# Optimization experiments

Hardware: AMD Instinct MI355X
Metric: run time of the kernel (lower is better)

The kernel has to match this reference:

```python
import jax, jax.numpy as jnp
import numpy as np

N = 262144
DX = 126
A_DIM = 2
IN = DX + A_DIM  # 128
Z = 10


def _bn(h, g, b):
    # torch BatchNorm1d in train mode: biased batch stats
    mu = h.mean(0)
    var = h.var(0)
    return g * (h - mu) * jax.lax.rsqrt(var + 1e-5) + b


def _kld(mu_p, ss_p, mu_q, ss_q):
    # KL between diagonal Gaussians per-sample, /dim, mean over batch
    k = mu_p.shape[1]
    kl = 0.5 * (jnp.sum(jnp.log(ss_q) - jnp.log(ss_p) + ss_p / ss_q
                        + (mu_p - mu_q) ** 2 / ss_q, axis=1) - k)
    return jnp.mean(kl / k)


def _sym(mu1, ss1, mu2, ss2):
    return 0.5 * (_kld(mu1, ss1, mu2, ss2) + _kld(mu2, ss2, mu1, ss1))


def _bce(p, t):
    return -jnp.mean(t * jnp.log(p) + (1.0 - t) * jnp.log(1.0 - p))


def _corr(x, y):
    n = x.shape[0]
    xm, ym = x.mean(), y.mean()
    xv = jnp.sum((x - xm) ** 2) / (n - 1)
    yv = jnp.sum((y - ym) ** 2) / (n - 1)
    c = jnp.abs(jnp.sum((x - xm) * (y - ym)) / jnp.sqrt(xv * yv))
    return jnp.where(xm == 0, 0.0, c)


def _twin(z, y, a):
    # fused segmented replacement for the python where/argmax group loops
    gid = y.astype(jnp.int32) * A_DIM + jnp.argmax(a, axis=1).astype(jnp.int32)
    G = 2 * A_DIM
    ones = jnp.ones((z.shape[0],), z.dtype)
    cnt = jax.ops.segment_sum(ones, gid, num_segments=G)
    s1 = jax.ops.segment_sum(z, gid, num_segments=G)
    s2 = jax.ops.segment_sum(z * z, gid, num_segments=G)
    safe = jnp.maximum(cnt, 1.0)[:, None]
    mean = s1 / safe
    var = (s2 - cnt[:, None] * mean ** 2) / jnp.maximum(cnt - 1.0, 1.0)[:, None]
    mean = mean.reshape(2, A_DIM, -1)
    var = var.reshape(2, A_DIM, -1)
    valid = (cnt >= 2).reshape(2, A_DIM)
    d = (jnp.sum((mean[:, :-1] - mean[:, 1:]) ** 2, -1)
         + jnp.sum((var[:, :-1] - var[:, 1:]) ** 2, -1))
    msk = valid[:, :-1] & valid[:, 1:]
    return jnp.sum(jnp.where(msk, d, 0.0))


def _forward(x, a, eps, y, p):
    (W1, b1, g1, be1, g2, be2, W2, b2,
     Wc1, bc1, Wc2, bc2, Wd1, bd1, Wd2, bd2, Wn, bnb) = p
    enc = lambda h: jax.nn.relu(_bn(jax.nn.relu(_bn(h @ W1 + b1, g1, be1)), g2, be2)) @ W2 + b2
    cla = lambda z: (z @ Wc1 + bc1) @ Wc2 + bc2
    dec = lambda z: (z @ Wd1 + bd1) @ Wd2 + bd2
    split = lambda zt: (zt[:, :10], zt[:, 10:20], zt[:, 20:30], zt[:, 30:40])

    def bi_kld(mx1, lx1, ms1, ls1, mx2, lx2, ms2, ls2):
        sx1, ss1 = jnp.exp(lx1), jnp.exp(ls1)
        sx2, ss2 = jnp.exp(lx2), jnp.exp(ls2)
        return (_sym(mx1, sx1, mx2, sx2), _sym(ms1, ss1, ms2, ss2),
                (_sym(mx1, sx1, ms1, ss1), _sym(mx2, sx2, ms2, ss2)))

    # pass 1: encoder on (x,a) / (x,1-a); only zx1/zx2 are used (for y_pred)
    mx1, ms1, lx1, ls1 = split(enc(jnp.concatenate([x, a], 1)))
    mx2, ms2, lx2, ls2 = split(enc(jnp.concatenate([x, 1.0 - a], 1)))
    zx1 = eps[0] * jnp.exp(lx1 / 2) + mx1
    zx2 = eps[2] * jnp.exp(lx2 / 2) + mx2
    y_pred = jnp.argmax(cla(zx1) + cla(zx2), axis=1).astype(x.dtype)[:, None]

    # pass 2: new_net then encoder
    out_o = jax.nn.relu(jnp.concatenate([x, a, y_pred], 1) @ Wn + bnb)
    out_c = jax.nn.relu(jnp.concatenate([x, 1.0 - a, y_pred], 1) @ Wn + bnb)
    mx1, ms1, lx1, ls1 = split(enc(out_o))
    mx2, ms2, lx2, ls2 = split(enc(out_c))
    d_zx, d_zs, (dxs1, dxs2) = bi_kld(mx1, lx1, ms1, ls1, mx2, lx2, ms2, ls2)
    zx1 = eps[4] * jnp.exp(lx1 / 2) + mx1
    zs1 = eps[5] * jnp.exp(ls1 / 2) + ms1
    zx2 = eps[6] * jnp.exp(lx2 / 2) + mx2
    zs2 = eps[7] * jnp.exp(ls2 / 2) + ms2

    r1 = jax.nn.sigmoid(dec(jnp.concatenate([zx1, zs1], 1)))
    r2 = jax.nn.sigmoid(dec(jnp.concatenate([zx2, zs2], 1)))
    x_ori, a_ori = jax.nn.sigmoid(x), jax.nn.sigmoid(a)
    recon_loss = (0.5 * (_bce(r1[:, :-A_DIM], x_ori) + _bce(r2[:, :-A_DIM], x_ori))
                  + 0.5 * (_bce(r1[:, -A_DIM:], a_ori) + _bce(r2[:, -A_DIM:], a_ori)))

    rs1 = jax.nn.sigmoid(dec(jnp.concatenate([zx1, zs2], 1)))
    rs2 = jax.nn.sigmoid(dec(jnp.concatenate([zx2, zs1], 1)))
    sr_loss = 0.5 * (_bce(rs1, jnp.concatenate([x_ori, a_ori], 1))
                     + _bce(rs2, jnp.concatenate([x_ori, jax.nn.sigmoid(1.0 - a)], 1)))

    dis_loss = d_zx + jnp.exp(-d_zs) + jnp.exp(-dxs1) + jnp.exp(-dxs2)
    twin = _twin(zx1, y, a)
    a_tags = jnp.argmax(a, 1).astype(x.dtype)
    yi = y.astype(jnp.int32)[:, None]
    ce = lambda lg: -jnp.take_along_axis(jax.nn.log_softmax(lg, -1), yi, axis=1)[:, 0]
    cl = 0.5 * (ce(cla(zx1)) + ce(cla(zx2)))
    F1 = 1.0  # config.f1
    return (jnp.sum(cl), F1 * _corr(a_tags, cl), 0.1 * twin,
            dis_loss, recon_loss, sr_loss)


def setup_inputs() -> dict:
    key = jax.random.key(0)
    ks = jax.random.split(key, 16)
    w = lambda k, shp: jax.random.normal(k, shp, jnp.float32) * 0.05
    return {
        'x': jax.random.normal(ks[0], (N, DX), jnp.float32),
        'a': jax.random.uniform(ks[1], (N, A_DIM), jnp.float32),
        'eps': jax.random.normal(ks[2], (8, N, Z), jnp.float32),
        'y': jax.random.randint(ks[3], (N,), 0, 2).astype(jnp.int32),
        'W1': w(ks[4], (IN, 128)), 'b1': jnp.zeros(128, jnp.float32),
        'g1': jnp.ones(128, jnp.float32), 'be1': jnp.zeros(128, jnp.float32),
        'g2': jnp.ones(128, jnp.float32), 'be2': jnp.zeros(128, jnp.float32),
        'W2': w(ks[5], (128, 40)), 'b2': jnp.zeros(40, jnp.float32),
        'Wc1': w(ks[6], (Z, 32)), 'bc1': jnp.zeros(32, jnp.float32),
        'Wc2': w(ks[7], (32, 2)), 'bc2': jnp.zeros(2, jnp.float32),
        'Wd1': w(ks[8], (20, 16)), 'bd1': jnp.zeros(16, jnp.float32),
        'Wd2': w(ks[9], (16, IN)), 'bd2': jnp.zeros(IN, jnp.float32),
        'Wn': w(ks[10], (IN + 1, IN)), 'bnb': jnp.zeros(IN, jnp.float32),
    }


def reference(x, a, eps, y, W1, b1, g1, be1, g2, be2, W2, b2,
              Wc1, bc1, Wc2, bc2, Wd1, bd1, Wd2, bd2, Wn, bnb):
    p = (W1, b1, g1, be1, g2, be2, W2, b2,
         Wc1, bc1, Wc2, bc2, Wd1, bd1, Wd2, bd2, Wn, bnb)
    return _forward(x, a, eps, y, p)
```

## Files before the change

kernel.cpp:

```cpp
#include <hip/hip_runtime.h>
#include <hip/hip_bf16.h>
#include <math.h>


#define N_      262144
#define DX_     126

static const size_t OFF_STATS = 0;
static const size_t OFF_PAR   = 32768;
static const size_t OFF_BUFA  = 65536;
static const size_t SZ_NH     = (size_t)N_ * 128 * 4;
static const size_t OFF_BUFB  = OFF_BUFA + SZ_NH;
static const size_t OFF_E1    = OFF_BUFB + SZ_NH;
static const size_t OFF_E2    = OFF_E1 + (size_t)N_*40*4;
static const size_t OFF_ZX1   = OFF_E2 + (size_t)N_*40*4;
static const size_t OFF_ZS1   = OFF_ZX1 + (size_t)N_*10*4;
static const size_t OFF_ZX2   = OFF_ZS1 + (size_t)N_*10*4;
static const size_t OFF_ZS2   = OFF_ZX2 + (size_t)N_*10*4;
static const size_t OFF_YP    = OFF_ZS2 + (size_t)N_*10*4;

#define ST_P1BN1    0
#define ST_P1BN2    512
#define ST_P2BN1    1024
#define ST_P2BN2    1536
#define ST_KLD      2048
#define ST_CL       2052
#define ST_TWIN_CNT 2056
#define ST_TWIN_S1  2060
#define ST_TWIN_S2  2100
#define ST_BCE_PART 2176

#define PP1BN1  0
#define PP1BN2  512
#define PP2BN1  1024
#define PP2BN2  1536

__device__ __forceinline__ float softplus_f(float u) {
    return fmaxf(u, 0.0f) + __logf(1.0f + __expf(-fabsf(u)));
}
__device__ __forceinline__ float sigmoid_f(float u) {
    return __builtin_amdgcn_rcpf(1.0f + __expf(-u));
}

#define BMg 128
#define BKg 32

__global__ __launch_bounds__(256, 4) void gemm_plain_kernel(
    const float* __restrict__ A, int K, const float* __restrict__ W,
    float* __restrict__ C)
{
    __shared__ __align__(16) float As[BKg][BMg + 4];
    __shared__ __align__(16) float Bs[BKg][128];
    const int row0 = blockIdx.x * BMg;
    const int tid  = threadIdx.x;
    const int tr   = (tid / 16) * 8;
    const int tc   = (tid % 16) * 8;
    float acc[8][8] = {};
    const int nk = (K + BKg - 1) / BKg;
    for (int kc = 0; kc < nk; ++kc) {
        const int k0 = kc * BKg;
        #pragma unroll
        for (int i = 0; i < 16; ++i) {
            int idx = tid + i * 256;
            int m = idx / BKg, k = idx % BKg;
            int gk = k0 + k;
            As[k][m] = (gk < K) ? A[(size_t)(row0 + m) * K + gk] : 0.0f;
        }
        #pragma unroll
        for (int i = 0; i < 16; ++i) {
            int idx = tid + i * 256;
            int k = idx / 128, n = idx % 128;
            int gk = k0 + k;
            Bs[k][n] = (gk < K) ? W[(size_t)gk * 128 + n] : 0.0f;
        }
        __syncthreads();
        #pragma unroll
        for (int k = 0; k < BKg; ++k) {
            float4 a0 = *(const float4*)&As[k][tr];
            float4 a1 = *(const float4*)&As[k][tr + 4];
            float4 b0 = *(const float4*)&Bs[k][tc];
            float4 b1v = *(const float4*)&Bs[k][tc + 4];
            float av[8] = {a0.x, a0.y, a0.z, a0.w, a1.x, a1.y, a1.z, a1.w};
            float bv[8] = {b0.x, b0.y, b0.z, b0.w, b1v.x, b1v.y, b1v.z, b1v.w};
            #pragma unroll
            for (int i = 0; i < 8; ++i)
                #pragma unroll
                for (int j = 0; j < 8; ++j)
                    acc[i][j] = fmaf(av[i], bv[j], acc[i][j]);
        }
        __syncthreads();
    }
    #pragma unroll
    for (int i = 0; i < 8; ++i) {
        float4 s0 = {acc[i][0], acc[i][1], acc[i][2], acc[i][3]};
        float4 s1 = {acc[i][4], acc[i][5], acc[i][6], acc[i][7]};
        size_t base = (size_t)(row0 + tr + i) * 128 + tc;
        *(float4*)&C[base]     = s0;
        *(float4*)&C[base + 4] = s1;
    }
}

__global__ __launch_bounds__(256, 4) void gemm_front_kernel(
    const float* U2, const float* __restrict__ a,
    const float* __restrict__ ypred, const float* __restrict__ Wn,
    const float* __restrict__ bnb, int conj,
    const float* __restrict__ W1, const float* __restrict__ b1,
    float* Cout)
{
    __shared__ __align__(16) float As[BKg][BMg + 4];
    __shared__ __align__(16) float Bs[BKg][128];
    __shared__ float ra0[BMg], ra1[BMg], ryp[BMg];
    __shared__ float w6s[128], w7s[128], w8s[128], bns[128];
    const int row0 = blockIdx.x * BMg;
    const int tid  = threadIdx.x;
    if (tid < 128) {
        int r = row0 + tid;
        float a0 = a[2 * r], a1 = a[2 * r + 1];
        if (conj) { a0 = 1.0f - a0; a1 = 1.0f - a1; }
        ra0[tid] = a0; ra1[tid] = a1; ryp[tid] = ypred[r];
        w6s[tid] = Wn[126 * 128 + tid];
        w7s[tid] = Wn[127 * 128 + tid];
        w8s[tid] = Wn[128 * 128 + tid];
        bns[tid] = bnb[tid];
    }
    __syncthreads();
    const int tr = (tid / 16) * 8;
    const int tc = (tid % 16) * 8;
    float acc[8][8] = {};
    for (int kc = 0; kc < 4; ++kc) {
        const int k0 = kc * BKg;
        #pragma unroll
        for (int i = 0; i < 16; ++i) {
            int idx = tid + i * 256;
            int m = idx / BKg, k = idx % BKg;
            int gk = k0 + k;
            float u = U2[(size_t)(row0 + m) * 128 + gk];
            float v = u + ra0[m] * w6s[gk] + ra1[m] * w7s[gk]
                        + ryp[m] * w8s[gk] + bns[gk];
            As[k][m] = fmaxf(v, 0.0f);
        }
        #pragma unroll
        for (int i = 0; i < 16; ++i) {
            int idx = tid + i * 256;
            int k = idx / 128, n = idx % 128;
            Bs[k][n] = W1[(size_t)(k0 + k) * 128 + n];
        }
        __syncthreads();
        #pragma unroll
        for (int k = 0; k < BKg; ++k) {
            float4 a0 = *(const float4*)&As[k][tr];
            float4 a1 = *(const float4*)&As[k][tr + 4];
            float4 b0 = *(const float4*)&Bs[k][tc];
            float4 b1v = *(const float4*)&Bs[k][tc + 4];
            float av[8] = {a0.x, a0.y, a0.z, a0.w, a1.x, a1.y, a1.z, a1.w};
            float bv[8] = {b0.x, b0.y, b0.z, b0.w, b1v.x, b1v.y, b1v.z, b1v.w};
            #pragma unroll
            for (int i = 0; i < 8; ++i)
                #pragma unroll
                for (int j = 0; j < 8; ++j)
                    acc[i][j] = fmaf(av[i], bv[j], acc[i][j]);
        }
        __syncthreads();
    }
    float bias[8];
    #pragma unroll
    for (int j = 0; j < 8; ++j) bias[j] = b1[tc + j];
    #pragma unroll
    for (int i = 0; i < 8; ++i) {
        float4 s0 = {acc[i][0] + bias[0], acc[i][1] + bias[1],
                     acc[i][2] + bias[2], acc[i][3] + bias[3]};
        float4 s1 = {acc[i][4] + bias[4], acc[i][5] + bias[5],
                     acc[i][6] + bias[6], acc[i][7] + bias[7]};
        size_t base = (size_t)(row0 + tr + i) * 128 + tc;
        *(float4*)&Cout[base]     = s0;
        *(float4*)&Cout[base + 4] = s1;
    }
}

__global__ __launch_bounds__(256) void stats_p1_bn1_kernel(
    const float* __restrict__ U1, const float* __restrict__ a,
    const float* __restrict__ W1, const float* __restrict__ b1,
    double* __restrict__ stat)
{
    const int tid = threadIdx.x;
    const int col = tid & 127, half = tid >> 7;
    const int r0 = blockIdx.x * 256 + half * 128;
    const float w6 = W1[126 * 128 + col], w7 = W1[127 * 128 + col];
    const float bb = b1[col];
    double dso = 0, dqo = 0, dsc = 0, dqc = 0;
    for (int i0 = 0; i0 < 128; i0 += 64) {
        float so = 0, qo = 0, sc = 0, qc = 0;
        for (int i = i0; i < i0 + 64; ++i) {
            int r = r0 + i;
            float u  = U1[(size_t)r * 128 + col];
            float a0 = a[2 * r], a1 = a[2 * r + 1];
            float ho = u + a0 * w6 + a1 * w7 + bb;
            float hc = u + (1.0f - a0) * w6 + (1.0f - a1) * w7 + bb;
            so += ho; qo += ho * ho; sc += hc; qc += hc * hc;
        }
        dso += so; dqo += qo; dsc += sc; dqc += qc;
    }
    __shared__ double red[4][128];
    if (half == 1) { red[0][col]=dso; red[1][col]=dqo; red[2][col]=dsc; red[3][col]=dqc; }
    __syncthreads();
    if (half == 0) {
        atomicAdd(&stat[col],       dso + red[0][col]);
        atomicAdd(&stat[128 + col], dqo + red[1][col]);
        atomicAdd(&stat[256 + col], dsc + red[2][col]);
        atomicAdd(&stat[384 + col], dqc + red[3][col]);
    }
}

__global__ __launch_bounds__(256) void stats_p1_bn2_kernel(
    const float* __restrict__ U1, const float* __restrict__ a,
    const float* __restrict__ W1, const float* __restrict__ b1,
    const float* __restrict__ Pbn1, double* __restrict__ stat)
{
    const int tid = threadIdx.x;
    const int col = tid & 127, half = tid >> 7;
    const int r0 = blockIdx.x * 256 + half * 128;
    const float w6 = W1[126 * 128 + col], w7 = W1[127 * 128 + col];
    const float bb = b1[col];
    const float A1o = Pbn1[col],       B1o = Pbn1[128 + col];
    const float A1c = Pbn1[256 + col], B1c = Pbn1[384 + col];
    double dso = 0, dqo = 0, dsc = 0, dqc = 0;
    for (int i0 = 0; i0 < 128; i0 += 64) {
        float so = 0, qo = 0, sc = 0, qc = 0;
        for (int i = i0; i < i0 + 64; ++i) {
            int r = r0 + i;
            float u  = U1[(size_t)r * 128 + col];
            float a0 = a[2 * r], a1 = a[2 * r + 1];
            float ho = u + a0 * w6 + a1 * w7 + bb;
            float hc = u + (1.0f - a0) * w6 + (1.0f - a1) * w7 + bb;
            float r1o = fmaxf(fmaf(A1o, ho, B1o), 0.0f);
            float r1c = fmaxf(fmaf(A1c, hc, B1c), 0.0f);
            so += r1o; qo += r1o * r1o; sc += r1c; qc += r1c * r1c;
        }
        dso += so; dqo += qo; dsc += sc; dqc += qc;
    }
    __shared__ double red[4][128];
    if (half == 1) { red[0][col]=dso; red[1][col]=dqo; red[2][col]=dsc; red[3][col]=dqc; }
    __syncthreads();
    if (half == 0) {
        atomicAdd(&stat[col],       dso + red[0][col]);
        atomicAdd(&stat[128 + col], dqo + red[1][col]);
        atomicAdd(&stat[256 + col], dsc + red[2][col]);
        atomicAdd(&stat[384 + col], dqc + red[3][col]);
    }
}

__global__ __launch_bounds__(256) void stats_p2_bn1_kernel(
    const float* __restrict__ H1o, const float* __restrict__ H1c,
    double* __restrict__ stat)
{
    const int tid = threadIdx.x;
    const int col = tid & 127, br = tid >> 7;
    const float* H = br ? H1c : H1o;
    const int r0 = blockIdx.x * 256;
    double ds = 0, dq = 0;
    for (int i0 = 0; i0 < 256; i0 += 64) {
        float s = 0, q = 0;
        for (int i = i0; i < i0 + 64; ++i) {
            float h = H[(size_t)(r0 + i) * 128 + col];
            s += h; q += h * h;
        }
        ds += s; dq += q;
    }
    atomicAdd(&stat[br * 256 + col], ds);
    atomicAdd(&stat[br * 256 + 128 + col], dq);
}

__global__ __launch_bounds__(256) void stats_p2_bn2_kernel(
    const float* __restrict__ H1o, const float* __restrict__ H1c,
    const float* __restrict__ Pbn1, double* __restrict__ stat)
{
    const int tid = threadIdx.x;
    const int col = tid & 127, br = tid >> 7;
    const float* H = br ? H1c : H1o;
    const float A1 = Pbn1[br * 256 + col], B1 = Pbn1[br * 256 + 128 + col];
    const int r0 = blockIdx.x * 256;
    double ds = 0, dq = 0;
    for (int i0 = 0; i0 < 256; i0 += 64) {
        float s = 0, q = 0;
        for (int i = i0; i < i0 + 64; ++i) {
            float h = H[(size_t)(r0 + i) * 128 + col];
            float r1 = fmaxf(fmaf(A1, h, B1), 0.0f);
            s += r1; q += r1 * r1;
        }
        ds += s; dq += q;
    }
    atomicAdd(&stat[br * 256 + col], ds);
    atomicAdd(&stat[br * 256 + 128 + col], dq);
}

__global__ void finalize_bn_kernel(const double* __restrict__ stat,
                                   const float* __restrict__ g,
                                   const float* __restrict__ be,
                                   float* __restrict__ Pout)
{
    const int br = blockIdx.x, j = threadIdx.x;
    double s = stat[br * 256 + j], q = stat[br * 256 + 128 + j];
    double mu = s / (double)N_;
    double var = q / (double)N_ - mu * mu;
    float rstd = (float)rsqrt(var + 1e-5);
    float A = g[j] * rstd;
    float B = be[j] - (float)mu * A;
    Pout[br * 256 + j] = A;
    Pout[br * 256 + 128 + j] = B;
}

__global__ __launch_bounds__(256) void tail_p1_kernel(
    const float* __restrict__ U1, const float* __restrict__ a, int conj,
    const float* __restrict__ W1, const float* __restrict__ b1,
    const float* __restrict__ A1p, const float* __restrict__ B1p,
    const float* __restrict__ A2p, const float* __restrict__ B2p,
    const float* __restrict__ W2, const float* __restrict__ b2,
    const float* __restrict__ epsk, float* __restrict__ zout)
{
    __shared__ float As[128][69];
    __shared__ float outs[64][24];
    const int row0 = blockIdx.x * 64;
    const int tid  = threadIdx.x;
    for (int i = tid; i < 64 * 128; i += 256) {
        int r = i >> 7, k = i & 127;
        int gr = row0 + r;
        float a0 = a[2 * gr], a1 = a[2 * gr + 1];
        if (conj) { a0 = 1.0f - a0; a1 = 1.0f - a1; }
        float h = U1[(size_t)gr * 128 + k] + a0 * W1[126 * 128 + k]
                + a1 * W1[127 * 128 + k] + b1[k];
        float r1 = fmaxf(fmaf(A1p[k], h, B1p[k]), 0.0f);
        float r2 = fmaxf(fmaf(A2p[k], r1, B2p[k]), 0.0f);
        As[k][r] = r2;
    }
    __syncthreads();
    const int row = tid & 63;
    const int cg  = tid >> 6;
    const int wbase = __builtin_amdgcn_readfirstlane((cg < 2) ? cg * 5 : 10 + cg * 5);
    float acc[5] = {};
    for (int k = 0; k < 128; ++k) {
        float av = As[k][row];
        #pragma unroll
        for (int c = 0; c < 5; ++c)
            acc[c] = fmaf(av, W2[k * 40 + wbase + c], acc[c]);
    }
    #pragma unroll
    for (int c = 0; c < 5; ++c)
        outs[row][cg * 5 + c] = acc[c] + b2[wbase + c];
    __syncthreads();
    if (tid < 128) {
        int r = tid & 63, dg = tid >> 6;
        int gr = row0 + r;
        #pragma unroll
        for (int c = 0; c < 5; ++c) {
            int d = dg * 5 + c;
            float mx = outs[r][d], lx = outs[r][10 + d];
            zout[(size_t)gr * 10 + d] =
                epsk[(size_t)gr * 10 + d] * __expf(0.5f * lx) + mx;
        }
    }
}

__global__ __launch_bounds__(256) void tail_p2_kernel(
    const float* __restrict__ H1,
    const float* __restrict__ A1p, const float* __restrict__ B1p,
    const float* __restrict__ A2p, const float* __restrict__ B2p,
    const float* __restrict__ W2, const float* __restrict__ b2,
    float* __restrict__ E)
{
    __shared__ float As[128][69];
    __shared__ float outs[64][44];
    const int row0 = blockIdx.x * 64;
    const int tid  = threadIdx.x;
    for (int i = tid; i < 64 * 128; i += 256) {
        int r = i >> 7, k = i & 127;
        float h = H1[(size_t)(row0 + r) * 128 + k];
        float r1 = fmaxf(fmaf(A1p[k], h, B1p[k]), 0.0f);
        float r2 = fmaxf(fmaf(A2p[k], r1, B2p[k]), 0.0f);
        As[k][r] = r2;
    }
    __syncthreads();
    const int row = tid & 63;
    const int cg  = tid >> 6;
    const int wbase = __builtin_amdgcn_readfirstlane(cg * 10);
    float acc[10] = {};
    for (int k = 0; k < 128; ++k) {
        float av = As[k][row];
        #pragma unroll
        for (int c = 0; c < 10; ++c)
            acc[c] = fmaf(av, W2[k * 40 + wbase + c], acc[c]);
    }
    #pragma unroll
    for (int c = 0; c < 10; ++c)
        outs[row][wbase + c] = acc[c] + b2[wbase + c];
    __syncthreads();
    size_t base = (size_t)row0 * 40;
    for (int i = tid; i < 64 * 40; i += 256)
        E[base + i] = outs[i / 40][i % 40];
}

__global__ __launch_bounds__(256) void cla_argmax_kernel(
    const float* __restrict__ zx1, const float* __restrict__ zx2,
    const float* __restrict__ Wc1, const float* __restrict__ bc1,
    const float* __restrict__ Wc2, const float* __restrict__ bc2,
    float* __restrict__ ypred)
{
    const int r = blockIdx.x * 256 + threadIdx.x;
    float z1[10], z2[10];
    #pragma unroll
    for (int d = 0; d < 10; ++d) {
        z1[d] = zx1[(size_t)r * 10 + d];
        z2[d] = zx2[(size_t)r * 10 + d];
    }
    float lg0 = 2.0f * bc2[0], lg1 = 2.0f * bc2[1];
    #pragma unroll
    for (int j = 0; j < 32; ++j) {
        float s1 = bc1[j], s2 = bc1[j];
        #pragma unroll
        for (int d = 0; d < 10; ++d) {
            float w = Wc1[d * 32 + j];
            s1 += z1[d] * w; s2 += z2[d] * w;
        }
        float s = s1 + s2;
        lg0 += s * Wc2[j * 2 + 0];
        lg1 += s * Wc2[j * 2 + 1];
    }
    ypred[r] = (lg1 > lg0) ? 1.0f : 0.0f;
}

__device__ __forceinline__ float sym10(const float* m1, const float* l1,
                                       const float* m2, const float* l2)
{
    float t12 = 0, t21 = 0;
    #pragma unroll
    for (int j = 0; j < 10; ++j) {
        float dl = l1[j] - l2[j];
        float md = m1[j] - m2[j]; md *= md;
        t12 += -dl + __expf(dl)  + md * __expf(-l2[j]);
        t21 +=  dl + __expf(-dl) + md * __expf(-l1[j]);
    }
    return 0.025f * ((t12 - 10.0f) + (t21 - 10.0f));
}

__device__ __forceinline__ float ce2_of(const float* z, int yv,
    const float* Wc1, const float* bc1, const float* Wc2, const float* bc2)
{
    float lg0 = bc2[0], lg1 = bc2[1];
    #pragma unroll
    for (int j = 0; j < 32; ++j) {
        float s = bc1[j];
        #pragma unroll
        for (int d = 0; d < 10; ++d) s += z[d] * Wc1[d * 32 + j];
        lg0 += s * Wc2[j * 2 + 0];
        lg1 += s * Wc2[j * 2 + 1];
    }
    float m = fmaxf(lg0, lg1);
    float lse = m + __logf(__expf(lg0 - m) + __expf(lg1 - m));
    float ly = yv ? lg1 : lg0;
    return -(ly - lse);
}

__global__ __launch_bounds__(256) void latents_kernel(
    const float* __restrict__ E1, const float* __restrict__ E2,
    const float* __restrict__ eps,
    const int* __restrict__ y, const float* __restrict__ a,
    const float* __restrict__ Wc1, const float* __restrict__ bc1,
    const float* __restrict__ Wc2, const float* __restrict__ bc2,
    float* __restrict__ zx1, float* __restrict__ zs1,
    float* __restrict__ zx2, float* __restrict__ zs2,
    double* __restrict__ stat)
{
    __shared__ float tw_cnt[4], tw_s1[40], tw_s2[40];
    __shared__ float redw[4][8];
    const int tid = threadIdx.x;
    if (tid < 4) tw_cnt[tid] = 0.0f;
    if (tid < 40) { tw_s1[tid] = 0.0f; tw_s2[tid] = 0.0f; }
    __syncthreads();

    const int r = blockIdx.x * 256 + tid;
    const size_t NS = (size_t)N_ * 10;
    float e1[40], e2[40];
    #pragma unroll
    for (int i = 0; i < 40; ++i) {
        e1[i] = E1[(size_t)r * 40 + i];
        e2[i] = E2[(size_t)r * 40 + i];
    }
    float s_dzx  = sym10(e1 + 0,  e1 + 20, e2 + 0,  e2 + 20);
    float s_dzs  = sym10(e1 + 10, e1 + 30, e2 + 10, e2 + 30);
    float s_dxs1 = sym10(e1 + 0,  e1 + 20, e1 + 10, e1 + 30);
    float s_dxs2 = sym10(e2 + 0,  e2 + 20, e2 + 10, e2 + 30);

    float z1[10], z2[10];
    #pragma unroll
    for (int d = 0; d < 10; ++d) {
        size_t rd = (size_t)r * 10 + d;
        float v1 = eps[4 * NS + rd] * __expf(0.5f * e1[20 + d]) + e1[d];
        float t1 = eps[5 * NS + rd] * __expf(0.5f * e1[30 + d]) + e1[10 + d];
        float v2 = eps[6 * NS + rd] * __expf(0.5f * e2[20 + d]) + e2[d];
        float t2 = eps[7 * NS + rd] * __expf(0.5f * e2[30 + d]) + e2[10 + d];
        zx1[rd] = v1; zs1[rd] = t1; zx2[rd] = v2; zs2[rd] = t2;
        z1[d] = v1; z2[d] = v2;
    }

    const int yv = y[r];
    float ce1 = ce2_of(z1, yv, Wc1, bc1, Wc2, bc2);
    float ce2 = ce2_of(z2, yv, Wc1, bc1, Wc2, bc2);
    float cl = 0.5f * (ce1 + ce2);
    float atag = (a[2 * r + 1] > a[2 * r]) ? 1.0f : 0.0f;

    int gid = yv * 2 + (int)atag;
    atomicAdd(&tw_cnt[gid], 1.0f);
    #pragma unroll
    for (int d = 0; d < 10; ++d) {
        atomicAdd(&tw_s1[gid * 10 + d], z1[d]);
        atomicAdd(&tw_s2[gid * 10 + d], z1[d] * z1[d]);
    }

    float vals[8] = {s_dzx, s_dzs, s_dxs1, s_dxs2, cl, cl * cl, atag * cl, atag};
    #pragma unroll
    for (int v = 0; v < 8; ++v) {
        float sv = vals[v];
        #pragma unroll
        for (int off = 1; off < 64; off <<= 1) sv += __shfl_xor(sv, off);
        vals[v] = sv;
    }
    const int wave = tid >> 6;
    if ((tid & 63) == 0) {
        #pragma unroll
        for (int v = 0; v < 8; ++v) redw[wave][v] = vals[v];
    }
    __syncthreads();
    if (tid < 8) {
        float s = redw[0][tid] + redw[1][tid] + redw[2][tid] + redw[3][tid];
        atomicAdd(&stat[ST_KLD + tid], (double)s);
    }
    if (tid < 4)  atomicAdd(&stat[ST_TWIN_CNT + tid], (double)tw_cnt[tid]);
    if (tid < 40) {
        atomicAdd(&stat[ST_TWIN_S1 + tid], (double)tw_s1[tid]);
        atomicAdd(&stat[ST_TWIN_S2 + tid], (double)tw_s2[tid]);
    }
}

#define DB_ROWS 32

__global__ __launch_bounds__(256) void dec_bce_kernel(
    const float* __restrict__ zx1, const float* __restrict__ zs1,
    const float* __restrict__ zx2, const float* __restrict__ zs2,
    const float* __restrict__ x, const float* __restrict__ a,
    const float* __restrict__ Wd1, const float* __restrict__ bd1,
    const float* __restrict__ Wd2, const float* __restrict__ bd2,
    double* __restrict__ stat)
{
    __shared__ float zsh[DB_ROWS][40];
    __shared__ float hsh[DB_ROWS][68];
    __shared__ float wsh[16 * 128];
    __shared__ float bsh[128];
    __shared__ float ash[DB_ROWS][2];
    __shared__ float redw[4][8];
    const int t = threadIdx.x;
    const int row0 = blockIdx.x * DB_ROWS;

    for (int i = t; i < DB_ROWS * 40; i += 256) {
        int rr = i / 40, d = i % 40;
        const float* src = (d < 10) ? zx1 : (d < 20) ? zs1 : (d < 30) ? zx2 : zs2;
        zsh[rr][d] = src[(size_t)(row0 + rr) * 10 + (d % 10)];
    }
    for (int i = t; i < 2048; i += 256) wsh[i] = Wd2[i];
    if (t < 128) bsh[t] = bd2[t];
    if (t < 64) { int rr = t >> 1, c = t & 1; ash[rr][c] = a[2 * (row0 + rr) + c]; }
    __syncthreads();

    for (int i = t; i < DB_ROWS * 64; i += 256) {
        int rr = i >> 6, ck = i & 63, c = ck >> 4, k = ck & 15;
        int oA = (c == 0 || c == 2) ? 0 : 20;
        int oB = (c == 0 || c == 3) ? 10 : 30;
        float s = bd1[k];
        #pragma unroll
        for (int d = 0; d < 10; ++d) {
            s = fmaf(zsh[rr][oA + d], Wd1[d * 16 + k], s);
            s = fmaf(zsh[rr][oB + d], Wd1[(10 + d) * 16 + k], s);
        }
        hsh[rr][c * 16 + k] = s;
    }
    __syncthreads();

    const int rloc = t >> 3, jl = t & 7;
    const int gr = row0 + rloc;
    float h0[16], h1[16], h2[16], h3[16];
    #pragma unroll
    for (int k = 0; k < 16; ++k) {
        h0[k] = hsh[rloc][k];      h1[k] = hsh[rloc][16 + k];
        h2[k] = hsh[rloc][32 + k]; h3[k] = hsh[rloc][48 + k];
    }
    const float a0 = ash[rloc][0], a1 = ash[rloc][1];
    float s1x = 0, s1a = 0, s2x = 0, s2a = 0, ss1 = 0, ss2 = 0;
    #pragma unroll 4
    for (int i = 0; i < 16; ++i) {
        const int j = jl + 8 * i;
        float u0 = bsh[j], u1 = bsh[j], u2 = bsh[j], u3 = bsh[j];
        #pragma unroll
        for (int k = 0; k < 16; ++k) {
            float w = wsh[k * 128 + j];
            u0 = fmaf(h0[k], w, u0); u1 = fmaf(h1[k], w, u1);
            u2 = fmaf(h2[k], w, u2); u3 = fmaf(h3[k], w, u3);
        }
        float sp0 = softplus_f(u0), sp1 = softplus_f(u1);
        float sp2 = softplus_f(u2), sp3 = softplus_f(u3);
        if (j < 126) {
            float tt = sigmoid_f(x[(size_t)gr * 126 + j]);
            s1x += sp0 - tt * u0; s2x += sp1 - tt * u1;
            ss1 += sp2 - tt * u2; ss2 += sp3 - tt * u3;
        } else {
            float av = (j == 126) ? a0 : a1;
            float tt = sigmoid_f(av);
            s1a += sp0 - tt * u0; s2a += sp1 - tt * u1;
            ss1 += sp2 - tt * u2;
            float t2 = sigmoid_f(1.0f - av);
            ss2 += sp3 - t2 * u3;
        }
    }

    float vals[6] = {s1x, s1a, s2x, s2a, ss1, ss2};
    #pragma unroll
    for (int v = 0; v < 6; ++v) {
        float sv = vals[v];
        #pragma unroll
        for (int off = 1; off < 64; off <<= 1) sv += __shfl_xor(sv, off);
        vals[v] = sv;
    }
    const int wave = t >> 6;
    if ((t & 63) == 0) {
        #pragma unroll
        for (int v = 0; v < 6; ++v) redw[wave][v] = vals[v];
    }
    __syncthreads();
    if (t < 6) {
        float s = redw[0][t] + redw[1][t] + redw[2][t] + redw[3][t];
        atomicAdd(&stat[ST_BCE_PART + t * 64 + (blockIdx.x & 63)], (double)s);
    }
}

__global__ void finalize_out_kernel(const double* __restrict__ st,
                                    float* __restrict__ out)
{
    if (threadIdx.x != 0 || blockIdx.x != 0) return;
    const double n = (double)N_;
    double bce[6];
    for (int v = 0; v < 6; ++v) {
        double s = 0;
        for (int b = 0; b < 64; ++b) s += st[ST_BCE_PART + v * 64 + b];
        bce[v] = s;
    }
    double dzx  = st[ST_KLD + 0] / n, dzs  = st[ST_KLD + 1] / n;
    double dxs1 = st[ST_KLD + 2] / n, dxs2 = st[ST_KLD + 3] / n;
    double Scl = st[ST_CL + 0], Scl2 = st[ST_CL + 1];
    double Sxcl = st[ST_CL + 2], Sx = st[ST_CL + 3];
    out[0] = (float)Scl;
    double xm = Sx / n, ym = Scl / n;
    double xv = (Sx - n * xm * xm) / (n - 1.0);
    double yv = (Scl2 - n * ym * ym) / (n - 1.0);
    double c  = fabs((Sxcl - n * xm * ym) / sqrt(xv * yv));
    out[1] = (float)((xm == 0.0) ? 0.0 : c);
    double tw = 0.0;
    for (int yy = 0; yy < 2; ++yy) {
        double c0 = st[ST_TWIN_CNT + yy * 2], c1 = st[ST_TWIN_CNT + yy * 2 + 1];
        double d = 0.0;
        for (int j = 0; j < 10; ++j) {
            double m0 = st[ST_TWIN_S1 + (yy * 2) * 10 + j]     / fmax(c0, 1.0);
            double m1 = st[ST_TWIN_S1 + (yy * 2 + 1) * 10 + j] / fmax(c1, 1.0);
            double w0 = (st[ST_TWIN_S2 + (yy * 2) * 10 + j]     - c0 * m0 * m0) / fmax(c0 - 1.0, 1.0);
            double w1 = (st[ST_TWIN_S2 + (yy * 2 + 1) * 10 + j] - c1 * m1 * m1) / fmax(c1 - 1.0, 1.0);
            d += (m0 - m1) * (m0 - m1) + (w0 - w1) * (w0 - w1);
        }
        if (c0 >= 2.0 && c1 >= 2.0) tw += d;
    }
    out[2] = (float)(0.1 * tw);
    out[3] = (float)(dzx + exp(-dzs) + exp(-dxs1) + exp(-dxs2));
    double recon = 0.5 * (bce[0] + bce[2]) / (n * 126.0)
                 + 0.5 * (bce[1] + bce[3]) / (n * 2.0);
    out[4] = (float)recon;
    out[5] = (float)(0.5 * (bce[4] + bce[5]) / (n * 128.0));
}

extern "C" void kernel_launch(void* const* d_in, const int* in_sizes, int n_in,
                              void* d_out, int out_size, void* d_ws, size_t ws_size,
                              hipStream_t stream)
{
    const float* x   = (const float*)d_in[0];
    const float* a   = (const float*)d_in[1];
    const float* eps = (const float*)d_in[2];
    const int*   y   = (const int*)d_in[3];
    const float* W1  = (const float*)d_in[4];
    const float* b1  = (const float*)d_in[5];
    const float* g1  = (const float*)d_in[6];
    const float* be1 = (const float*)d_in[7];
    const float* g2  = (const float*)d_in[8];
    const float* be2 = (const float*)d_in[9];
    const float* W2  = (const float*)d_in[10];
    const float* b2  = (const float*)d_in[11];
    const float* Wc1 = (const float*)d_in[12];
    const float* bc1 = (const float*)d_in[13];
    const float* Wc2 = (const float*)d_in[14];
    const float* bc2 = (const float*)d_in[15];
    const float* Wd1 = (const float*)d_in[16];
    const float* bd1 = (const float*)d_in[17];
    const float* Wd2 = (const float*)d_in[18];
    const float* bd2 = (const float*)d_in[19];
    const float* Wn  = (const float*)d_in[20];
    const float* bnb = (const float*)d_in[21];

    char* ws = (char*)d_ws;
    double* st  = (double*)(ws + OFF_STATS);
    float* P    = (float*)(ws + OFF_PAR);
    float* bufA = (float*)(ws + OFF_BUFA);
    float* bufB = (float*)(ws + OFF_BUFB);
    float* E1   = (float*)(ws + OFF_E1);
    float* E2   = (float*)(ws + OFF_E2);
    float* zx1  = (float*)(ws + OFF_ZX1);
    float* zs1  = (float*)(ws + OFF_ZS1);
    float* zx2  = (float*)(ws + OFF_ZX2);
    float* zs2  = (float*)(ws + OFF_ZS2);
    float* yp   = (float*)(ws + OFF_YP);
    const size_t NS = (size_t)N_ * 10;

    hipMemsetAsync(st, 0, 32768, stream);

    gemm_plain_kernel<<<N_ / 128, 256, 0, stream>>>(x, DX_, W1, bufA);
    gemm_plain_kernel<<<N_ / 128, 256, 0, stream>>>(x, DX_, Wn, bufB);
    stats_p1_bn1_kernel<<<1024, 256, 0, stream>>>(bufA, a, W1, b1, st + ST_P1BN1);
    finalize_bn_kernel<<<2, 128, 0, stream>>>(st + ST_P1BN1, g1, be1, P + PP1BN1);
    stats_p1_bn2_kernel<<<1024, 256, 0, stream>>>(bufA, a, W1, b1, P + PP1BN1, st + ST_P1BN2);
    finalize_bn_kernel<<<2, 128, 0, stream>>>(st + ST_P1BN2, g2, be2, P + PP1BN2);
    tail_p1_kernel<<<N_ / 64, 256, 0, stream>>>(bufA, a, 0, W1, b1,
        P + PP1BN1, P + PP1BN1 + 128, P + PP1BN2, P + PP1BN2 + 128,
        W2, b2, eps + 0 * NS, zx1);
    tail_p1_kernel<<<N_ / 64, 256, 0, stream>>>(bufA, a, 1, W1, b1,
        P + PP1BN1 + 256, P + PP1BN1 + 384, P + PP1BN2 + 256, P + PP1BN2 + 384,
        W2, b2, eps + 2 * NS, zx2);
    cla_argmax_kernel<<<N_ / 256, 256, 0, stream>>>(zx1, zx2, Wc1, bc1, Wc2, bc2, yp);

    gemm_front_kernel<<<N_ / 128, 256, 0, stream>>>(bufB, a, yp, Wn, bnb, 0, W1, b1, bufA);
    gemm_front_kernel<<<N_ / 128, 256, 0, stream>>>(bufB, a, yp, Wn, bnb, 1, W1, b1, bufB);
    stats_p2_bn1_kernel<<<1024, 256, 0, stream>>>(bufA, bufB, st + ST_P2BN1);
    finalize_bn_kernel<<<2, 128, 0, stream>>>(st + ST_P2BN1, g1, be1, P + PP2BN1);
    stats_p2_bn2_kernel<<<1024, 256, 0, stream>>>(bufA, bufB, P + PP2BN1, st + ST_P2BN2);
    finalize_bn_kernel<<<2, 128, 0, stream>>>(st + ST_P2BN2, g2, be2, P + PP2BN2);
    tail_p2_kernel<<<N_ / 64, 256, 0, stream>>>(bufA,
        P + PP2BN1, P + PP2BN1 + 128, P + PP2BN2, P + PP2BN2 + 128, W2, b2, E1);
    tail_p2_kernel<<<N_ / 64, 256, 0, stream>>>(bufB,
        P + PP2BN1 + 256, P + PP2BN1 + 384, P + PP2BN2 + 256, P + PP2BN2 + 384, W2, b2, E2);
    latents_kernel<<<N_ / 256, 256, 0, stream>>>(E1, E2, eps, y, a,
        Wc1, bc1, Wc2, bc2, zx1, zs1, zx2, zs2, st);
    dec_bce_kernel<<<N_ / DB_ROWS, 256, 0, stream>>>(zx1, zs1, zx2, zs2, x, a,
        Wd1, bd1, Wd2, bd2, st);
    finalize_out_kernel<<<1, 64, 0, stream>>>(st, (float*)d_out);
}
```

Measured before the change: 2.755 ms.

## Fuse paired GEMMs and fold BN1 statistics into GEMM epilogues

The two x-projections (W1 and Wn) become one kernel that loads each x tile once and computes both products. The two front GEMMs (original and conjugate action) become one kernel that shares the W1 tile. Both kernels now compute the BN1 sum and sum-of-squares in their epilogue through a shared-memory reduction followed by double atomics, so the separate stats passes that re-read the full hidden buffers are removed. The cost is smaller 64-row tiles, higher register and LDS use, lower occupancy, and many more atomics per launch.

Measured after the change: 2.613 ms. -5.1%, faster.

```diff
diff --git a/kernel.cpp b/kernel.cpp
--- a/kernel.cpp
+++ b/kernel.cpp
@@ -42,173 +42,203 @@
     return __builtin_amdgcn_rcpf(1.0f + __expf(-u));
 }
 
-#define BMg 128
 #define BKg 32
 
-__global__ __launch_bounds__(256, 4) void gemm_plain_kernel(
-    const float* __restrict__ A, int K, const float* __restrict__ W,
-    float* __restrict__ C)
-{
-    __shared__ __align__(16) float As[BKg][BMg + 4];
-    __shared__ __align__(16) float Bs[BKg][128];
-    const int row0 = blockIdx.x * BMg;
+#define REDUCE_STAT(vec, off)                                        \
+    __syncthreads();                                                 \
+    _Pragma("unroll")                                                \
+    for (int j = 0; j < 4; ++j) red[rg][tc + j] = vec[j];            \
+    __syncthreads();                                                 \
+    if (tid < 128) {                                                 \
+        float tsum = 0.0f;                                           \
+        _Pragma("unroll")                                            \
+        for (int g = 0; g < 8; ++g) tsum += red[g][tid];             \
+        atomicAdd(&stat[(off) + tid], (double)tsum);                 \
+    }
+
+__global__ __launch_bounds__(256, 3) void gemm_dual_kernel(
+    const float* __restrict__ A, const float* __restrict__ W1,
+    const float* __restrict__ Wn, const float* __restrict__ a,
+    const float* __restrict__ b1,
+    float* __restrict__ C1, float* __restrict__ C2,
+    double* __restrict__ stat)
+{
+    __shared__ __align__(16) float As[BKg][68];
+    __shared__ __align__(16) float B1s[BKg][128];
+    __shared__ __align__(16) float B2s[BKg][128];
+    __shared__ float red[8][128];
+    const int row0 = blockIdx.x * 64;
     const int tid  = threadIdx.x;
-    const int tr   = (tid / 16) * 8;
-    const int tc   = (tid % 16) * 8;
-    float acc[8][8] = {};
-    const int nk = (K + BKg - 1) / BKg;
-    for (int kc = 0; kc < nk; ++kc) {
-        const int k0 = kc * BKg;
+    const int tr   = (tid >> 5) * 8;
+    const int tc   = (tid & 31) * 4;
+    const int rg   = tid >> 5;
+    float acc1[8][4] = {}, acc2[8][4] = {};
+    for (int kc = 0; kc < 4; ++kc) {
+        const int k0 = kc * 32;
+        #pragma unroll
+        for (int i = 0; i < 8; ++i) {
+            int idx = tid + i * 256;
+            int m = idx >> 5, k = idx & 31;
+            int gk = k0 + k;
+            As[k][m] = (gk < DX_) ? A[(size_t)(row0 + m) * DX_ + gk] : 0.0f;
+        }
         #pragma unroll
         for (int i = 0; i < 16; ++i) {
             int idx = tid + i * 256;
-            int m = idx / BKg, k = idx % BKg;
+            int k = idx >> 7, n = idx & 127;
             int gk = k0 + k;
-            As[k][m] = (gk < K) ? A[(size_t)(row0 + m) * K + gk] : 0.0f;
-        }
-        #pragma unroll
-        for (int i = 0; i < 16; ++i) {
-            int idx = tid + i * 256;
-            int k = idx / 128, n = idx % 128;
-            int gk = k0 + k;
-            Bs[k][n] = (gk < K) ? W[(size_t)gk * 128 + n] : 0.0f;
+            B1s[k][n] = (gk < DX_) ? W1[(size_t)gk * 128 + n] : 0.0f;
+            B2s[k][n] = (gk < DX_) ? Wn[(size_t)gk * 128 + n] : 0.0f;
         }
         __syncthreads();
         #pragma unroll
         for (int k = 0; k < BKg; ++k) {
-            float4 a0 = *(const float4*)&As[k][tr];
-            float4 a1 = *(const float4*)&As[k][tr + 4];
-            float4 b0 = *(const float4*)&Bs[k][tc];
-            float4 b1v = *(const float4*)&Bs[k][tc + 4];
-            float av[8] = {a0.x, a0.y, a0.z, a0.w, a1.x, a1.y, a1.z, a1.w};
-            float bv[8] = {b0.x, b0.y, b0.z, b0.w, b1v.x, b1v.y, b1v.z, b1v.w};
+            float4 av0 = *(const float4*)&As[k][tr];
+            float4 av1 = *(const float4*)&As[k][tr + 4];
+            float4 bv1 = *(const float4*)&B1s[k][tc];
+            float4 bv2 = *(const float4*)&B2s[k][tc];
+            float av[8] = {av0.x, av0.y, av0.z, av0.w, av1.x, av1.y, av1.z, av1.w};
+            float w1v[4] = {bv1.x, bv1.y, bv1.z, bv1.w};
+            float w2v[4] = {bv2.x, bv2.y, bv2.z, bv2.w};
             #pragma unroll
             for (int i = 0; i < 8; ++i)
                 #pragma unroll
-                for (int j = 0; j < 8; ++j)
-                    acc[i][j] = fmaf(av[i], bv[j], acc[i][j]);
+                for (int j = 0; j < 4; ++j) {
+                    acc1[i][j] = fmaf(av[i], w1v[j], acc1[i][j]);
+                    acc2[i][j] = fmaf(av[i], w2v[j], acc2[i][j]);
+                }
         }
         __syncthreads();
     }
     #pragma unroll
     for (int i = 0; i < 8; ++i) {
-        float4 s0 = {acc[i][0], acc[i][1], acc[i][2], acc[i][3]};
-        float4 s1 = {acc[i][4], acc[i][5], acc[i][6], acc[i][7]};
         size_t base = (size_t)(row0 + tr + i) * 128 + tc;
-        *(float4*)&C[base]     = s0;
-        *(float4*)&C[base + 4] = s1;
-    }
-}
-
-__global__ __launch_bounds__(256, 4) void gemm_front_kernel(
+        float4 v1 = {acc1[i][0], acc1[i][1], acc1[i][2], acc1[i][3]};
+        float4 v2 = {acc2[i][0], acc2[i][1], acc2[i][2], acc2[i][3]};
+        *(float4*)&C1[base] = v1;
+        *(float4*)&C2[base] = v2;
+    }
+    float w6[4], w7[4], bb[4];
+    #pragma unroll
+    for (int j = 0; j < 4; ++j) {
+        w6[j] = W1[126 * 128 + tc + j];
+        w7[j] = W1[127 * 128 + tc + j];
+        bb[j] = b1[tc + j];
+    }
+    float ra0[8], ra1[8];
+    #pragma unroll
+    for (int i = 0; i < 8; ++i) {
+        ra0[i] = a[2 * (row0 + tr + i)];
+        ra1[i] = a[2 * (row0 + tr + i) + 1];
+    }
+    float s_ho[4] = {}, q_ho[4] = {}, s_hc[4] = {}, q_hc[4] = {};
+    #pragma unroll
+    for (int i = 0; i < 8; ++i)
+        #pragma unroll
+        for (int j = 0; j < 4; ++j) {
+            float u  = acc1[i][j];
+            float ho = u + ra0[i] * w6[j] + ra1[i] * w7[j] + bb[j];
+            float hc = u + (1.0f - ra0[i]) * w6[j] + (1.0f - ra1[i]) * w7[j] + bb[j];
+            s_ho[j] += ho; q_ho[j] += ho * ho;
+            s_hc[j] += hc; q_hc[j] += hc * hc;
+        }
+    REDUCE_STAT(s_ho, 0)
+    REDUCE_STAT(q_ho, 128)
+    REDUCE_STAT(s_hc, 256)
+    REDUCE_STAT(q_hc, 384)
+}
+
+__global__ __launch_bounds__(256, 3) void gemm_front_dual_kernel(
     const float* U2, const float* __restrict__ a,
     const float* __restrict__ ypred, const float* __restrict__ Wn,
-    const float* __restrict__ bnb, int conj,
+    const float* __restrict__ bnb,
     const float* __restrict__ W1, const float* __restrict__ b1,
-    float* Cout)
-{
-    __shared__ __align__(16) float As[BKg][BMg + 4];
+    float* __restrict__ H1o, float* H1c,
+    double* __restrict__ stat)
+{
+    __shared__ __align__(16) float Ao[BKg][68];
+    __shared__ __align__(16) float Ac[BKg][68];
     __shared__ __align__(16) float Bs[BKg][128];
-    __shared__ float ra0[BMg], ra1[BMg], ryp[BMg];
-    __shared__ float w6s[128], w7s[128], w8s[128], bns[128];
-    const int row0 = blockIdx.x * BMg;
+    __shared__ float red[8][128];
+    __shared__ float sa0[64], sa1[64], syp[64];
+    const int row0 = blockIdx.x * 64;
     const int tid  = threadIdx.x;
-    if (tid < 128) {
+    if (tid < 64) {
         int r = row0 + tid;
-        float a0 = a[2 * r], a1 = a[2 * r + 1];
-        if (conj) { a0 = 1.0f - a0; a1 = 1.0f - a1; }
-        ra0[tid] = a0; ra1[tid] = a1; ryp[tid] = ypred[r];
-        w6s[tid] = Wn[126 * 128 + tid];
-        w7s[tid] = Wn[127 * 128 + tid];
-        w8s[tid] = Wn[128 * 128 + tid];
-        bns[tid] = bnb[tid];
-    }
-    __syncthreads();
-    const int tr = (tid / 16) * 8;
-    const int tc = (tid % 16) * 8;
-    float acc[8][8] = {};
+        sa0[tid] = a[2 * r]; sa1[tid] = a[2 * r + 1]; syp[tid] = ypred[r];
+    }
+    __syncthreads();
+    const int tr = (tid >> 5) * 8;
+    const int tc = (tid & 31) * 4;
+    const int rg = tid >> 5;
+    float acco[8][4] = {}, accc[8][4] = {};
     for (int kc = 0; kc < 4; ++kc) {
-        const int k0 = kc * BKg;
+        const int k0 = kc * 32;
+        #pragma unroll
+        for (int i = 0; i < 8; ++i) {
+            int idx = tid + i * 256;
+            int m = idx >> 5, k = idx & 31;
+            int gk = k0 + k;
+            float u  = U2[(size_t)(row0 + m) * 128 + gk];
+            float w6 = Wn[126 * 128 + gk], w7 = Wn[127 * 128 + gk];
+            float w8 = Wn[128 * 128 + gk];
+            float vb = u + syp[m] * w8 + bnb[gk];
+            float vo = vb + sa0[m] * w6 + sa1[m] * w7;
+            float vc = vb + (1.0f - sa0[m]) * w6 + (1.0f - sa1[m]) * w7;
+            Ao[k][m] = fmaxf(vo, 0.0f);
+            Ac[k][m] = fmaxf(vc, 0.0f);
+        }
         #pragma unroll
         for (int i = 0; i < 16; ++i) {
             int idx = tid + i * 256;
-            int m = idx / BKg, k = idx % BKg;
-            int gk = k0 + k;
-            float u = U2[(size_t)(row0 + m) * 128 + gk];
-            float v = u + ra0[m] * w6s[gk] + ra1[m] * w7s[gk]
-                        + ryp[m] * w8s[gk] + bns[gk];
-            As[k][m] = fmaxf(v, 0.0f);
-        }
-        #pragma unroll
-        for (int i = 0; i < 16; ++i) {
-            int idx = tid + i * 256;
-            int k = idx / 128, n = idx % 128;
+            int k = idx >> 7, n = idx & 127;
             Bs[k][n] = W1[(size_t)(k0 + k) * 128 + n];
         }
         __syncthreads();
         #pragma unroll
         for (int k = 0; k < BKg; ++k) {
-            float4 a0 = *(const float4*)&As[k][tr];
-            float4 a1 = *(const float4*)&As[k][tr + 4];
-            float4 b0 = *(const float4*)&Bs[k][tc];
-            float4 b1v = *(const float4*)&Bs[k][tc + 4];
-            float av[8] = {a0.x, a0.y, a0.z, a0.w, a1.x, a1.y, a1.z, a1.w};
-            float bv[8] = {b0.x, b0.y, b0.z, b0.w, b1v.x, b1v.y, b1v.z, b1v.w};
+            float4 ao0 = *(const float4*)&Ao[k][tr];
+            float4 ao1 = *(const float4*)&Ao[k][tr + 4];
+            float4 ac0 = *(const float4*)&Ac[k][tr];
+            float4 ac1 = *(const float4*)&Ac[k][tr + 4];
+            float4 bv  = *(const float4*)&Bs[k][tc];
+            float aov[8] = {ao0.x, ao0.y, ao0.z, ao0.w, ao1.x, ao1.y, ao1.z, ao1.w};
+            float acv[8] = {ac0.x, ac0.y, ac0.z, ac0.w, ac1.x, ac1.y, ac1.z, ac1.w};
+            float bvv[4] = {bv.x, bv.y, bv.z, bv.w};
             #pragma unroll
             for (int i = 0; i < 8; ++i)
                 #pragma unroll
-                for (int j = 0; j < 8; ++j)
-                    acc[i][j] = fmaf(av[i], bv[j], acc[i][j]);
+                for (int j = 0; j < 4; ++j) {
+                    acco[i][j] = fmaf(aov[i], bvv[j], acco[i][j]);
+                    accc[i][j] = fmaf(acv[i], bvv[j], accc[i][j]);
+                }
         }
         __syncthreads();
     }
-    float bias[8];
-    #pragma unroll
-    for (int j = 0; j < 8; ++j) bias[j] = b1[tc + j];
+    float bb[4];
+    #pragma unroll
+    for (int j = 0; j < 4; ++j) bb[j] = b1[tc + j];
+    float s_o[4] = {}, q_o[4] = {}, s_c[4] = {}, q_c[4] = {};
     #pragma unroll
     for (int i = 0; i < 8; ++i) {
-        float4 s0 = {acc[i][0] + bias[0], acc[i][1] + bias[1],
-                     acc[i][2] + bias[2], acc[i][3] + bias[3]};
-        float4 s1 = {acc[i][4] + bias[4], acc[i][5] + bias[5],
-                     acc[i][6] + bias[6], acc[i][7] + bias[7]};
+        float ho[4], hc[4];
+        #pragma unroll
+        for (int j = 0; j < 4; ++j) {
+            ho[j] = acco[i][j] + bb[j];
+            hc[j] = accc[i][j] + bb[j];
+            s_o[j] += ho[j]; q_o[j] += ho[j] * ho[j];
+            s_c[j] += hc[j]; q_c[j] += hc[j] * hc[j];
+        }
         size_t base = (size_t)(row0 + tr + i) * 128 + tc;
-        *(float4*)&Cout[base]     = s0;
-        *(float4*)&Cout[base + 4] = s1;
-    }
-}
-
-__global__ __launch_bounds__(256) void stats_p1_bn1_kernel(
-    const float* __restrict__ U1, const float* __restrict__ a,
-    const float* __restrict__ W1, const float* __restrict__ b1,
-    double* __restrict__ stat)
-{
-    const int tid = threadIdx.x;
-    const int col = tid & 127, half = tid >> 7;
-    const int r0 = blockIdx.x * 256 + half * 128;
-    const float w6 = W1[126 * 128 + col], w7 = W1[127 * 128 + col];
-    const float bb = b1[col];
-    double dso = 0, dqo = 0, dsc = 0, dqc = 0;
-    for (int i0 = 0; i0 < 128; i0 += 64) {
-        float so = 0, qo = 0, sc = 0, qc = 0;
-        for (int i = i0; i < i0 + 64; ++i) {
-            int r = r0 + i;
-            float u  = U1[(size_t)r * 128 + col];
-            float a0 = a[2 * r], a1 = a[2 * r + 1];
-            float ho = u + a0 * w6 + a1 * w7 + bb;
-            float hc = u + (1.0f - a0) * w6 + (1.0f - a1) * w7 + bb;
-            so += ho; qo += ho * ho; sc += hc; qc += hc * hc;
-        }
-        dso += so; dqo += qo; dsc += sc; dqc += qc;
-    }
-    __shared__ double red[4][128];
-    if (half == 1) { red[0][col]=dso; red[1][col]=dqo; red[2][col]=dsc; red[3][col]=dqc; }
-    __syncthreads();
-    if (half == 0) {
-        atomicAdd(&stat[col],       dso + red[0][col]);
-        atomicAdd(&stat[128 + col], dqo + red[1][col]);
-        atomicAdd(&stat[256 + col], dsc + red[2][col]);
-        atomicAdd(&stat[384 + col], dqc + red[3][col]);
-    }
+        float4 vo4 = {ho[0], ho[1], ho[2], ho[3]};
+        float4 vc4 = {hc[0], hc[1], hc[2], hc[3]};
+        *(float4*)&H1o[base] = vo4;
+        *(float4*)&H1c[base] = vc4;
+    }
+    REDUCE_STAT(s_o, 0)
+    REDUCE_STAT(q_o, 128)
+    REDUCE_STAT(s_c, 256)
+    REDUCE_STAT(q_c, 384)
 }
 
 __global__ __launch_bounds__(256) void stats_p1_bn2_kernel(
@@ -247,27 +277,6 @@
         atomicAdd(&stat[256 + col], dsc + red[2][col]);
         atomicAdd(&stat[384 + col], dqc + red[3][col]);
     }
-}
-
-__global__ __launch_bounds__(256) void stats_p2_bn1_kernel(
-    const float* __restrict__ H1o, const float* __restrict__ H1c,
-    double* __restrict__ stat)
-{
-    const int tid = threadIdx.x;
-    const int col = tid & 127, br = tid >> 7;
-    const float* H = br ? H1c : H1o;
-    const int r0 = blockIdx.x * 256;
-    double ds = 0, dq = 0;
-    for (int i0 = 0; i0 < 256; i0 += 64) {
-        float s = 0, q = 0;
-        for (int i = i0; i < i0 + 64; ++i) {
-            float h = H[(size_t)(r0 + i) * 128 + col];
-            s += h; q += h * h;
-        }
-        ds += s; dq += q;
-    }
-    atomicAdd(&stat[br * 256 + col], ds);
-    atomicAdd(&stat[br * 256 + 128 + col], dq);
 }
 
 __global__ __launch_bounds__(256) void stats_p2_bn2_kernel(
@@ -724,9 +733,8 @@
 
     hipMemsetAsync(st, 0, 32768, stream);
 
-    gemm_plain_kernel<<<N_ / 128, 256, 0, stream>>>(x, DX_, W1, bufA);
-    gemm_plain_kernel<<<N_ / 128, 256, 0, stream>>>(x, DX_, Wn, bufB);
-    stats_p1_bn1_kernel<<<1024, 256, 0, stream>>>(bufA, a, W1, b1, st + ST_P1BN1);
+    gemm_dual_kernel<<<N_ / 64, 256, 0, stream>>>(x, W1, Wn, a, b1,
+        bufA, bufB, st + ST_P1BN1);
     finalize_bn_kernel<<<2, 128, 0, stream>>>(st + ST_P1BN1, g1, be1, P + PP1BN1);
     stats_p1_bn2_kernel<<<1024, 256, 0, stream>>>(bufA, a, W1, b1, P + PP1BN1, st + ST_P1BN2);
     finalize_bn_kernel<<<2, 128, 0, stream>>>(st + ST_P1BN2, g2, be2, P + PP1BN2);
@@ -738,9 +746,8 @@
         W2, b2, eps + 2 * NS, zx2);
     cla_argmax_kernel<<<N_ / 256, 256, 0, stream>>>(zx1, zx2, Wc1, bc1, Wc2, bc2, yp);
 
-    gemm_front_kernel<<<N_ / 128, 256, 0, stream>>>(bufB, a, yp, Wn, bnb, 0, W1, b1, bufA);
-    gemm_front_kernel<<<N_ / 128, 256, 0, stream>>>(bufB, a, yp, Wn, bnb, 1, W1, b1, bufB);
-    stats_p2_bn1_kernel<<<1024, 256, 0, stream>>>(bufA, bufB, st + ST_P2BN1);
+    gemm_front_dual_kernel<<<N_ / 64, 256, 0, stream>>>(bufB, a, yp, Wn, bnb,
+        W1, b1, bufA, bufB, st + ST_P2BN1);
     finalize_bn_kernel<<<2, 128, 0, stream>>>(st + ST_P2BN1, g1, be1, P + PP2BN1);
     stats_p2_bn2_kernel<<<1024, 256, 0, stream>>>(bufA, bufB, P + PP2BN1, st + ST_P2BN2);
     finalize_bn_kernel<<<2, 128, 0, stream>>>(st + ST_P2BN2, g2, be2, P + PP2BN2);
```
